# Optimization experiments

Measured on AMD Instinct MI355X. Metric: run time of the kernel, lower is better.

The kernel has to match this reference:

```python
import jax, jax.numpy as jnp
import numpy as np
from jax import lax

N_ITERS = 3
NUM_CAPS_IN = 768   # 32 * 4 * 6
NUM_CAPS_OUT = 64
CAPS_DIM_IN = 8
CAPS_DIM_OUT = 16


def _conv2d(x, w, b, stride):
    # x: NCHW, w: OIHW, VALID padding
    y = lax.conv_general_dilated(x, w, (stride, stride), 'VALID',
                                 dimension_numbers=('NCHW', 'OIHW', 'NCHW'))
    return y + b[None, :, None, None]


def _squash(x, axis):
    # norm**2 / (1 + norm**2) * x / norm  (as in the torch source)
    norm = jnp.linalg.norm(x, axis=axis, keepdims=True)
    return (norm ** 2) / (1.0 + norm ** 2) * x / norm


def setup_inputs() -> dict:
    key = jax.random.key(0)
    ks = jax.random.split(key, 4)
    B = 128
    x = jax.random.normal(ks[0], (B, 3, 32, 42), dtype=jnp.float32)
    conv1_w = jax.random.normal(ks[1], (32, 3, 6, 6), dtype=jnp.float32) * 0.1
    conv1_b = jnp.zeros((32,), dtype=jnp.float32)
    pc_w = jax.random.normal(ks[2], (256, 32, 3, 3), dtype=jnp.float32) * 0.1
    pc_b = jnp.zeros((256,), dtype=jnp.float32)
    # FinalCapsule W: (num_caps_in, num_caps_out, caps_dim_out, caps_dim_in)
    route_w = jax.random.normal(ks[3], (NUM_CAPS_IN, NUM_CAPS_OUT, CAPS_DIM_OUT, CAPS_DIM_IN), dtype=jnp.float32)
    return {"x": x, "conv1_w": conv1_w, "conv1_b": conv1_b,
            "pc_w": pc_w, "pc_b": pc_b, "route_w": route_w}


def reference(x, conv1_w, conv1_b, pc_w, pc_b, route_w):
    B = x.shape[0]
    # conv1: k=6, s=3 -> (B,32,9,13)
    h = jax.nn.relu(_conv2d(x, conv1_w, conv1_b, 3))
    # primary capsules: k=3, s=2 -> (B,256,4,6) -> (B,768,8)
    h = _conv2d(h, pc_w, pc_b, 2)
    u = h.reshape(B, -1, CAPS_DIM_IN)
    u = _squash(u, axis=-1)
    # prediction vectors: W[i,o,:,:] @ u[b,i,:] -> xh (B, 768, 64, 16)
    xh = jnp.einsum('iokd,bid->biok', route_w, u)
    xhd = lax.stop_gradient(xh)
    b_logits = jnp.zeros((B, NUM_CAPS_IN, NUM_CAPS_OUT), dtype=xh.dtype)
    for _ in range(N_ITERS - 1):
        c = jax.nn.softmax(b_logits, axis=2)                      # (B,768,64)
        s = jnp.sum(c[..., None] * xhd, axis=1, keepdims=True)   # (B,1,64,16)
        v = _squash(s, axis=-1)
        b_logits = b_logits + jnp.sum(xhd * v, axis=-1)
    c = jax.nn.softmax(b_logits, axis=2)
    s = jnp.sum(c[..., None] * xh, axis=1, keepdims=True)
    v = _squash(s, axis=-1)                                       # (B,1,64,16)
    return v[:, 0].reshape(B, NUM_CAPS_OUT * CAPS_DIM_OUT)        # (B,1024)
```

## Files before the change

kernel.cpp:

```cpp
#include <hip/hip_runtime.h>
#include <math.h>

typedef __attribute__((ext_vector_type(8))) short bfrag;
typedef __attribute__((ext_vector_type(4))) float f32x4;
typedef __attribute__((ext_vector_type(16))) float f32x16;
typedef __attribute__((ext_vector_type(4))) unsigned short ushort4v;

__device__ __forceinline__ void split8(const float* x, bfrag& hi, bfrag& lo) {
    #pragma unroll
    for (int j = 0; j < 8; ++j) {
        unsigned xb = __float_as_uint(x[j]);
        unsigned hb = xb & 0xffff0000u;
        float lf = x[j] - __uint_as_float(hb);
        hi[j] = (short)(xb >> 16);
        lo[j] = (short)(__float_as_uint(lf) >> 16);
    }
}
__device__ __forceinline__ void trunc8(const float* x, bfrag& hi) {
    #pragma unroll
    for (int j = 0; j < 8; ++j) hi[j] = (short)(__float_as_uint(x[j]) >> 16);
}

__global__ __launch_bounds__(256) void front_kernel(
    const float* __restrict__ x, const float* __restrict__ w1,
    const float* __restrict__ b1, float* __restrict__ B2) {
    __shared__ float xl[4032];
    __shared__ float wl[3456];
    __shared__ float hl[3744];
    int b = blockIdx.x, tid = threadIdx.x;
    const float* xb = x + (size_t)b * 4032;
    #pragma unroll
    for (int i = 0; i < 4; ++i) {
        int idx = tid + 256 * i;
        if (idx < 1008) *(float4*)(xl + idx * 4) = *(const float4*)(xb + idx * 4);
        if (idx < 864)  *(float4*)(wl + idx * 4) = *(const float4*)(w1 + idx * 4);
    }
    __syncthreads();
    for (int idx = tid; idx < 3744; idx += 256) {
        int oc = idx / 117, r = idx % 117;
        int oh = r / 13, ow = r % 13;
        float acc = b1[oc];
        #pragma unroll
        for (int ic = 0; ic < 3; ++ic) {
            const float* xc = xl + ic * 1344 + (oh * 3) * 42 + ow * 3;
            const float* wc = wl + (oc * 3 + ic) * 36;
            #pragma unroll
            for (int kh = 0; kh < 6; ++kh)
                #pragma unroll
                for (int kw = 0; kw < 6; ++kw)
                    acc += xc[kh * 42 + kw] * wc[kh * 6 + kw];
        }
        hl[idx] = fmaxf(acc, 0.f);
    }
    __syncthreads();
    for (int f = tid; f < 864; f += 256) {
        int ko = f / 24, s = f % 24;
        int h = s / 6, w = s % 6;
        float o8[8];
        #pragma unroll
        for (int j = 0; j < 8; ++j) {
            int k = ko * 8 + j;
            int ic = k / 9, rr = k % 9;
            int kh = rr / 3, kw = rr % 3;
            o8[j] = hl[ic * 117 + (2 * h + kh) * 13 + (2 * w + kw)];
        }
        float* dst = B2 + ((size_t)ko * 3072 + b * 24 + s) * 8;
        *(float4*)dst = *(const float4*)o8;
        *(float4*)(dst + 4) = *(const float4*)(o8 + 4);
    }
}

__global__ __launch_bounds__(256) void pc_gemm_kernel(
    const float* __restrict__ wpc, const float* __restrict__ bias,
    const float* __restrict__ B2, float* __restrict__ u2) {
    int wv = threadIdx.x >> 6;
    int l = threadIdx.x & 63;
    int q = l >> 4, r16 = l & 15;
    int c2t = blockIdx.y * 4 + wv;
    int n0 = blockIdx.x * 16;
    f32x4 acc = {0.f, 0.f, 0.f, 0.f};
    const float* ap0 = wpc + (size_t)(c2t * 16 + r16) * 288 + q * 8;
    const float* bp0 = B2 + ((size_t)q * 3072 + n0 + r16) * 8;
    #pragma unroll
    for (int ks = 0; ks < 9; ++ks) {
        float av[8], bv[8];
        *(float4*)av = *(const float4*)(ap0 + ks * 32);
        *(float4*)(av + 4) = *(const float4*)(ap0 + ks * 32 + 4);
        *(float4*)bv = *(const float4*)(bp0 + (size_t)ks * 98304);
        *(float4*)(bv + 4) = *(const float4*)(bp0 + (size_t)ks * 98304 + 4);
        bfrag ahi, alo, bhi, blo;
        split8(av, ahi, alo);
        split8(bv, bhi, blo);
        acc = __builtin_amdgcn_mfma_f32_16x16x32_bf16(ahi, bhi, acc, 0, 0, 0);
        acc = __builtin_amdgcn_mfma_f32_16x16x32_bf16(ahi, blo, acc, 0, 0, 0);
        acc = __builtin_amdgcn_mfma_f32_16x16x32_bf16(alo, bhi, acc, 0, 0, 0);
    }
    int n = n0 + r16;
    int b = n / 24, s = n % 24;
    float vals[4], n2[4];
    #pragma unroll
    for (int r = 0; r < 4; ++r) {
        float xv = acc[r] + bias[c2t * 16 + q * 4 + r];
        vals[r] = xv;
        n2[r] = xv * xv;
    }
    #pragma unroll
    for (int r = 0; r < 4; ++r) {
        n2[r] += __shfl_xor(n2[r], 1, 64);
        n2[r] += __shfl_xor(n2[r], 2, 64);
        n2[r] += __shfl_xor(n2[r], 4, 64);
    }
    #pragma unroll
    for (int r = 0; r < 4; ++r) {
        int c2 = c2t * 16 + q * 4 + r;
        int cap = c2 * 3 + (s >> 3);
        int d = s & 7;
        float nr = sqrtf(n2[r]);
        u2[((size_t)(cap * 2 + (d >> 2)) * 128 + b) * 4 + (d & 3)]
            = vals[r] * nr / (1.f + n2[r]);
    }
}

__global__ __launch_bounds__(128) void zsum_kernel(
    const float* __restrict__ blog, float* __restrict__ zsum) {
    int i = blockIdx.x;
    int b = threadIdx.x;
    const float* src = blog + (size_t)i * 128 + b;
    float sum = 0.f;
    #pragma unroll
    for (int o = 0; o < 64; ++o) sum += __expf(src[(size_t)o * 98304]);
    zsum[i * 128 + b] = sum;
}

template <bool UNIFORM>
__global__ __launch_bounds__(256, 4) void spass_kernel(
    const float* __restrict__ W, const float* __restrict__ u2,
    const float* __restrict__ blog, const float* __restrict__ zsum,
    float* __restrict__ s_part) {
    int o = blockIdx.x;
    int it = blockIdx.y;
    int tid = threadIdx.x;
    int wv = tid >> 6;
    int l = tid & 63;
    int q = l >> 4, r16 = l & 15;
    int i0 = it * 64;
    __shared__ unsigned short whi[64 * 136];
    __shared__ unsigned short wlo[64 * 136];

    float4 ua[3][2][2];
    float blv[3][2], zv[3][2];
    auto issue = [&](int s, int buf) {
        int cap = i0 + s * 4 + q;
        #pragma unroll
        for (int m = 0; m < 2; ++m) {
            int b = wv * 32 + m * 16 + r16;
            ua[buf][m][0] = *(const float4*)(u2 + ((size_t)(cap * 2 + 0) * 128 + b) * 4);
            ua[buf][m][1] = *(const float4*)(u2 + ((size_t)(cap * 2 + 1) * 128 + b) * 4);
            if (!UNIFORM) {
                blv[buf][m] = blog[((size_t)o * 768 + cap) * 128 + b];
                zv[buf][m]  = zsum[cap * 128 + b];
            }
        }
    };

    issue(0, 0);
    issue(1, 1);
    #pragma unroll
    for (int itr = 0; itr < 8; ++itr) {
        int F = tid + 256 * itr;
        int cap = F >> 5, slot = F & 31;
        float4 t4 = *(const float4*)(W + ((size_t)(i0 + cap) * 64 + o) * 128 + slot * 4);
        ushort4v h4, l4;
        float tf[4] = {t4.x, t4.y, t4.z, t4.w};
        #pragma unroll
        for (int j = 0; j < 4; ++j) {
            unsigned xb = __float_as_uint(tf[j]);
            float lf = tf[j] - __uint_as_float(xb & 0xffff0000u);
            h4[j] = (unsigned short)(xb >> 16);
            l4[j] = (unsigned short)(__float_as_uint(lf) >> 16);
        }
        *(ushort4v*)(whi + cap * 136 + slot * 4) = h4;
        *(ushort4v*)(wlo + cap * 136 + slot * 4) = l4;
    }
    __syncthreads();

    f32x4 acc0 = {0.f, 0.f, 0.f, 0.f};
    f32x4 acc1 = {0.f, 0.f, 0.f, 0.f};
    #pragma unroll
    for (int s = 0; s < 16; ++s) {
        int cur = s % 3;
        if (s < 14) issue(s + 2, (s + 2) % 3);
        int wrow = (s * 4 + q) * 136 + r16 * 8;
        bfrag bhi = *(const bfrag*)(whi + wrow);
        bfrag blo = *(const bfrag*)(wlo + wrow);
        #pragma unroll
        for (int m = 0; m < 2; ++m) {
            float uv[8];
            *(float4*)(uv) = ua[cur][m][0];
            *(float4*)(uv + 4) = ua[cur][m][1];
            if (!UNIFORM) {
                float c = __expf(blv[cur][m]) / zv[cur][m];
                #pragma unroll
                for (int j = 0; j < 8; ++j) uv[j] *= c;
            }
            bfrag ahi;
            trunc8(uv, ahi);
            if (m == 0) {
                acc0 = __builtin_amdgcn_mfma_f32_16x16x32_bf16(ahi, bhi, acc0, 0, 0, 0);
                acc0 = __builtin_amdgcn_mfma_f32_16x16x32_bf16(ahi, blo, acc0, 0, 0, 0);
            } else {
                acc1 = __builtin_amdgcn_mfma_f32_16x16x32_bf16(ahi, bhi, acc1, 0, 0, 0);
                acc1 = __builtin_amdgcn_mfma_f32_16x16x32_bf16(ahi, blo, acc1, 0, 0, 0);
            }
        }
    }
    #pragma unroll
    for (int reg = 0; reg < 4; ++reg) {
        int b0 = wv * 32 + q * 4 + reg;
        s_part[(((size_t)it * 128 + b0) * 64 + o) * 16 + r16] = acc0[reg];
        s_part[(((size_t)it * 128 + b0 + 16) * 64 + o) * 16 + r16] = acc1[reg];
    }
}

template <bool TRANSPOSED>
__global__ __launch_bounds__(256) void squashv_kernel(
    const float* __restrict__ s_part, float* __restrict__ v, float scale) {
    int idx = blockIdx.x * 256 + threadIdx.x;
    float acc = 0.f;
    #pragma unroll
    for (int it = 0; it < 12; ++it) acc += s_part[(size_t)it * 131072 + idx];
    acc *= scale;
    float n2 = acc * acc;
    n2 += __shfl_xor(n2, 1, 64);
    n2 += __shfl_xor(n2, 2, 64);
    n2 += __shfl_xor(n2, 4, 64);
    n2 += __shfl_xor(n2, 8, 64);
    float n = sqrtf(n2);
    float val = acc * n / (1.f + n2);
    if (TRANSPOSED) {
        int k = idx & 15, o = (idx >> 4) & 63, b = idx >> 10;
        v[((size_t)o * 128 + b) * 16 + k] = val;
    } else {
        v[idx] = val;
    }
}

template <bool ACCUM>
__global__ __launch_bounds__(256, 4) void bpass_kernel(
    const float* __restrict__ W, const float* __restrict__ u2,
    const float* __restrict__ v_t, float* __restrict__ blog) {
    int o = blockIdx.x, it = blockIdx.y;
    int tid = threadIdx.x;
    int wv = tid >> 6;
    int l = tid & 63;
    int r = l & 31;
    int kh = l >> 5;
    int capB = it * 32;
    __shared__ float wl[32 * 164];
    #pragma unroll
    for (int itr = 0; itr < 4; ++itr) {
        int F = tid + 256 * itr;
        int cap = F >> 5, slot = F & 31;
        int k = slot >> 1, dh = slot & 1;
        float4 t4 = *(const float4*)(W + ((size_t)(capB + cap) * 64 + o) * 128 + k * 8 + dh * 4);
        float* dst = wl + cap * 164 + (dh * 4) * 20 + k;
        dst[0] = t4.x; dst[20] = t4.y; dst[40] = t4.z; dst[60] = t4.w;
    }
    bfrag vhi[4], vlo[4];
    #pragma unroll
    for (int nt = 0; nt < 4; ++nt) {
        const float* vp = v_t + ((size_t)o * 128 + nt * 32 + r) * 16 + kh * 8;
        float vv8[8];
        *(float4*)(vv8) = *(const float4*)vp;
        *(float4*)(vv8 + 4) = *(const float4*)(vp + 4);
        split8(vv8, vhi[nt], vlo[nt]);
    }
    __syncthreads();
    #pragma unroll
    for (int mt = 0; mt < 2; ++mt) {
        int cl = wv * 8 + mt * 4 + (r >> 3);
        const float* ap = wl + cl * 164 + (r & 7) * 20 + kh * 8;
        float a8[8];
        *(float4*)(a8) = *(const float4*)ap;
        *(float4*)(a8 + 4) = *(const float4*)(ap + 4);
        int capg = capB + wv * 8 + mt * 4;
        int gw = kh * 2;
        float prevv[4][2];
        if (ACCUM) {
            #pragma unroll
            for (int nt = 0; nt < 4; ++nt) {
                int b = nt * 32 + r;
                #pragma unroll
                for (int gg = 0; gg < 2; ++gg)
                    prevv[nt][gg] = blog[((size_t)o * 768 + capg + gw + gg) * 128 + b];
            }
        }
        float4 u4b[2][4];
        #pragma unroll
        for (int g = 0; g < 4; ++g)
            u4b[0][g] = *(const float4*)(u2 + ((size_t)((capg + g) * 2 + kh) * 128 + r) * 4);
        bfrag ahi, alo;
        split8(a8, ahi, alo);
        #pragma unroll
        for (int nt = 0; nt < 4; ++nt) {
            int cur = nt & 1;
            if (nt < 3) {
                int bn = (nt + 1) * 32 + r;
                #pragma unroll
                for (int g = 0; g < 4; ++g)
                    u4b[cur ^ 1][g] = *(const float4*)(u2 + ((size_t)((capg + g) * 2 + kh) * 128 + bn) * 4);
            }
            int b = nt * 32 + r;
            f32x16 acc;
            #pragma unroll
            for (int z = 0; z < 16; ++z) acc[z] = 0.f;
            acc = __builtin_amdgcn_mfma_f32_32x32x16_bf16(ahi, vhi[nt], acc, 0, 0, 0);
            acc = __builtin_amdgcn_mfma_f32_32x32x16_bf16(ahi, vlo[nt], acc, 0, 0, 0);
            acc = __builtin_amdgcn_mfma_f32_32x32x16_bf16(alo, vhi[nt], acc, 0, 0, 0);
            float full[4];
            #pragma unroll
            for (int g = 0; g < 4; ++g) {
                float part = u4b[cur][g].x * acc[g * 4 + 0] + u4b[cur][g].y * acc[g * 4 + 1]
                           + u4b[cur][g].z * acc[g * 4 + 2] + u4b[cur][g].w * acc[g * 4 + 3];
                full[g] = part + __shfl_xor(part, 32, 64);
            }
            #pragma unroll
            for (int gg = 0; gg < 2; ++gg) {
                int g = gw + gg;
                size_t bi = ((size_t)o * 768 + capg + g) * 128 + b;
                blog[bi] = (ACCUM ? prevv[nt][gg] : 0.f) + full[g];
            }
        }
    }
}

extern "C" void kernel_launch(void* const* d_in, const int* in_sizes, int n_in,
                              void* d_out, int out_size, void* d_ws, size_t ws_size,
                              hipStream_t stream) {
    const float* x  = (const float*)d_in[0];
    const float* w1 = (const float*)d_in[1];
    const float* b1 = (const float*)d_in[2];
    const float* wp = (const float*)d_in[3];
    const float* bp = (const float*)d_in[4];
    const float* W  = (const float*)d_in[5];
    float* out = (float*)d_out;
    float* ws = (float*)d_ws;

    float* u2     = ws;
    float* blog   = ws + 786432;
    float* zsum   = ws + 7077888;
    float* v      = ws + 7274496;
    float* s_part = ws + 7405568;
    float* B2     = s_part;

    front_kernel<<<128, 256, 0, stream>>>(x, w1, b1, B2);
    pc_gemm_kernel<<<dim3(192, 4), 256, 0, stream>>>(wp, bp, B2, u2);

    spass_kernel<true><<<dim3(64, 12), 256, 0, stream>>>(W, u2, nullptr, nullptr, s_part);
    squashv_kernel<true><<<512, 256, 0, stream>>>(s_part, v, 1.f / 64.f);
    bpass_kernel<false><<<dim3(64, 24), 256, 0, stream>>>(W, u2, v, blog);

    zsum_kernel<<<768, 128, 0, stream>>>(blog, zsum);
    spass_kernel<false><<<dim3(64, 12), 256, 0, stream>>>(W, u2, blog, zsum, s_part);
    squashv_kernel<true><<<512, 256, 0, stream>>>(s_part, v, 1.f);
    bpass_kernel<true><<<dim3(64, 24), 256, 0, stream>>>(W, u2, v, blog);

    zsum_kernel<<<768, 128, 0, stream>>>(blog, zsum);
    spass_kernel<false><<<dim3(64, 12), 256, 0, stream>>>(W, u2, blog, zsum, s_part);
    squashv_kernel<false><<<512, 256, 0, stream>>>(s_part, out, 1.f);
}
```

Measured before the change: 141.1 us.

## Fuse partial-sum reduction and squash into bpass, drop intermediate squashv launches

Changes the s_part layout to o-major, then folds the 12-way partial-sum reduction and squash into the bpass prologue, which removes two squashv launches and the v buffer round trip. zsum now splits the 64 outputs across two threads per batch element and combines them with a shuffle. The cost is that each bpass block redundantly re-reduces 12 partials for its o, so there is more L2 traffic per block in exchange for fewer launches.

```diff
diff --git a/kernel.cpp b/kernel.cpp
--- a/kernel.cpp
+++ b/kernel.cpp
@@ -121,15 +121,17 @@
     }
 }
 
-__global__ __launch_bounds__(128) void zsum_kernel(
+__global__ __launch_bounds__(256) void zsum_kernel(
     const float* __restrict__ blog, float* __restrict__ zsum) {
     int i = blockIdx.x;
-    int b = threadIdx.x;
-    const float* src = blog + (size_t)i * 128 + b;
+    int tid = threadIdx.x;
+    int b = tid >> 1, oh = tid & 1;
+    const float* src = blog + (size_t)oh * 32 * 98304 + (size_t)i * 128 + b;
     float sum = 0.f;
     #pragma unroll
-    for (int o = 0; o < 64; ++o) sum += __expf(src[(size_t)o * 98304]);
-    zsum[i * 128 + b] = sum;
+    for (int o = 0; o < 32; ++o) sum += __expf(src[(size_t)o * 98304]);
+    sum += __shfl_xor(sum, 1, 64);
+    if (!oh) zsum[i * 128 + b] = sum;
 }
 
 template <bool UNIFORM>
@@ -217,38 +219,32 @@
     #pragma unroll
     for (int reg = 0; reg < 4; ++reg) {
         int b0 = wv * 32 + q * 4 + reg;
-        s_part[(((size_t)it * 128 + b0) * 64 + o) * 16 + r16] = acc0[reg];
-        s_part[(((size_t)it * 128 + b0 + 16) * 64 + o) * 16 + r16] = acc1[reg];
-    }
-}
-
-template <bool TRANSPOSED>
-__global__ __launch_bounds__(256) void squashv_kernel(
-    const float* __restrict__ s_part, float* __restrict__ v, float scale) {
+        s_part[(size_t)it * 131072 + o * 2048 + b0 * 16 + r16] = acc0[reg];
+        s_part[(size_t)it * 131072 + o * 2048 + (b0 + 16) * 16 + r16] = acc1[reg];
+    }
+}
+
+__global__ __launch_bounds__(256) void squashv_final(
+    const float* __restrict__ s_part, float* __restrict__ out) {
     int idx = blockIdx.x * 256 + threadIdx.x;
+    int k = idx & 15, o = (idx >> 4) & 63, b = idx >> 10;
+    const float* sp = s_part + o * 2048 + b * 16 + k;
     float acc = 0.f;
     #pragma unroll
-    for (int it = 0; it < 12; ++it) acc += s_part[(size_t)it * 131072 + idx];
-    acc *= scale;
+    for (int it = 0; it < 12; ++it) acc += sp[(size_t)it * 131072];
     float n2 = acc * acc;
     n2 += __shfl_xor(n2, 1, 64);
     n2 += __shfl_xor(n2, 2, 64);
     n2 += __shfl_xor(n2, 4, 64);
     n2 += __shfl_xor(n2, 8, 64);
     float n = sqrtf(n2);
-    float val = acc * n / (1.f + n2);
-    if (TRANSPOSED) {
-        int k = idx & 15, o = (idx >> 4) & 63, b = idx >> 10;
-        v[((size_t)o * 128 + b) * 16 + k] = val;
-    } else {
-        v[idx] = val;
-    }
+    out[idx] = acc * n / (1.f + n2);
 }
 
 template <bool ACCUM>
 __global__ __launch_bounds__(256, 4) void bpass_kernel(
     const float* __restrict__ W, const float* __restrict__ u2,
-    const float* __restrict__ v_t, float* __restrict__ blog) {
+    const float* __restrict__ s_part, float* __restrict__ blog, float scale) {
     int o = blockIdx.x, it = blockIdx.y;
     int tid = threadIdx.x;
     int wv = tid >> 6;
@@ -269,11 +265,25 @@
     bfrag vhi[4], vlo[4];
     #pragma unroll
     for (int nt = 0; nt < 4; ++nt) {
-        const float* vp = v_t + ((size_t)o * 128 + nt * 32 + r) * 16 + kh * 8;
-        float vv8[8];
-        *(float4*)(vv8) = *(const float4*)vp;
-        *(float4*)(vv8 + 4) = *(const float4*)(vp + 4);
-        split8(vv8, vhi[nt], vlo[nt]);
+        int b = nt * 32 + r;
+        const float* sp = s_part + o * 2048 + b * 16 + kh * 8;
+        float a8[8] = {0.f, 0.f, 0.f, 0.f, 0.f, 0.f, 0.f, 0.f};
+        #pragma unroll
+        for (int it2 = 0; it2 < 12; ++it2) {
+            float4 p0 = *(const float4*)(sp + (size_t)it2 * 131072);
+            float4 p1 = *(const float4*)(sp + (size_t)it2 * 131072 + 4);
+            a8[0] += p0.x; a8[1] += p0.y; a8[2] += p0.z; a8[3] += p0.w;
+            a8[4] += p1.x; a8[5] += p1.y; a8[6] += p1.z; a8[7] += p1.w;
+        }
+        float n2p = 0.f;
+        #pragma unroll
+        for (int j = 0; j < 8; ++j) { a8[j] *= scale; n2p += a8[j] * a8[j]; }
+        float n2 = n2p + __shfl_xor(n2p, 32, 64);
+        float nr = sqrtf(n2);
+        float sc = nr / (1.f + n2);
+        #pragma unroll
+        for (int j = 0; j < 8; ++j) a8[j] *= sc;
+        split8(a8, vhi[nt], vlo[nt]);
     }
     __syncthreads();
     #pragma unroll
@@ -349,7 +359,6 @@
     float* u2     = ws;
     float* blog   = ws + 786432;
     float* zsum   = ws + 7077888;
-    float* v      = ws + 7274496;
     float* s_part = ws + 7405568;
     float* B2     = s_part;
 
@@ -357,15 +366,13 @@
     pc_gemm_kernel<<<dim3(192, 4), 256, 0, stream>>>(wp, bp, B2, u2);
 
     spass_kernel<true><<<dim3(64, 12), 256, 0, stream>>>(W, u2, nullptr, nullptr, s_part);
-    squashv_kernel<true><<<512, 256, 0, stream>>>(s_part, v, 1.f / 64.f);
-    bpass_kernel<false><<<dim3(64, 24), 256, 0, stream>>>(W, u2, v, blog);
-
-    zsum_kernel<<<768, 128, 0, stream>>>(blog, zsum);
+    bpass_kernel<false><<<dim3(64, 24), 256, 0, stream>>>(W, u2, s_part, blog, 1.f / 64.f);
+
+    zsum_kernel<<<768, 256, 0, stream>>>(blog, zsum);
     spass_kernel<false><<<dim3(64, 12), 256, 0, stream>>>(W, u2, blog, zsum, s_part);
-    squashv_kernel<true><<<512, 256, 0, stream>>>(s_part, v, 1.f);
-    bpass_kernel<true><<<dim3(64, 24), 256, 0, stream>>>(W, u2, v, blog);
-
-    zsum_kernel<<<768, 128, 0, stream>>>(blog, zsum);
+    bpass_kernel<true><<<dim3(64, 24), 256, 0, stream>>>(W, u2, s_part, blog, 1.f);
+
+    zsum_kernel<<<768, 256, 0, stream>>>(blog, zsum);
     spass_kernel<false><<<dim3(64, 12), 256, 0, stream>>>(W, u2, blog, zsum, s_part);
-    squashv_kernel<false><<<512, 256, 0, stream>>>(s_part, out, 1.f);
-}
+    squashv_final<<<512, 256, 0, stream>>>(s_part, out);
+}
```

After: 201.3 us. +42.6%, slower.
